# Performance work log

Measured on AMD Instinct MI355X. Metric: run time of the kernel, lower is better.

The kernel has to match this reference:

```python
import jax, jax.numpy as jnp
import numpy as np

N_HEAD = 12
HEAD_SIZE = 64  # 768 / 12
SCALE = 1.0 / np.sqrt(HEAD_SIZE)


def setup_inputs() -> dict:
    key = jax.random.key(0)
    k1, k2, k3 = jax.random.split(key, 3)
    B, T, C = 8, 1024, 768
    x = jax.random.normal(k1, (B, T, C), dtype=jnp.float32)
    W_attn = jax.random.normal(k2, (C, 3 * C), dtype=jnp.float32) * 0.02
    b_attn = jax.random.normal(k3, (3 * C,), dtype=jnp.float32) * 0.02
    return {"x": x, "W_attn": W_attn, "b_attn": b_attn}


def reference(x, W_attn, b_attn):
    B, T, C = x.shape
    hs = C // N_HEAD
    qkv = x @ W_attn + b_attn                      # [B, T, 3C]
    q, k, v = jnp.split(qkv, 3, axis=-1)
    # [B, nh, T, hs]
    q = q.reshape(B, T, N_HEAD, hs).transpose(0, 2, 1, 3)
    k = k.reshape(B, T, N_HEAD, hs).transpose(0, 2, 1, 3)
    v = v.reshape(B, T, N_HEAD, hs).transpose(0, 2, 1, 3)
    scores = jnp.einsum('bhqd,bhkd->bhqk', q, k) * SCALE
    causal = jnp.tril(jnp.ones((T, T), dtype=bool))  # [T, T]
    # masked positions get -inf then relu -> 0; equivalent to where(mask, relu, 0)
    att = jnp.where(causal, jax.nn.relu(scores), 0.0)
    y = jnp.einsum('bhqk,bhkd->bhqd', att, v)      # [B, nh, T, hs]
    return y.transpose(0, 2, 1, 3).reshape(B, T, C)
```

## Files before the change

kernel.cpp:

```cpp
#include <hip/hip_runtime.h>
#include <stdint.h>

typedef __bf16 bf16;
typedef __attribute__((ext_vector_type(8))) __bf16 bf16x8;
typedef __attribute__((ext_vector_type(4))) __bf16 bf16x4;
typedef __attribute__((ext_vector_type(4))) float  f32x4;

#define ATT_SCALE 0.125f

__device__ __forceinline__ void async16(void* lds, const void* g) {
  __builtin_amdgcn_global_load_lds(
      (__attribute__((address_space(1))) void*)(void*)g,
      (__attribute__((address_space(3))) void*)lds,
      16, 0, 0);
}

__global__ void convert_x_kernel(const float* __restrict__ x, bf16* __restrict__ y) {
  size_t i = ((size_t)blockIdx.x * 256 + threadIdx.x) * 8;
  float4 a = *(const float4*)(x + i);
  float4 b = *(const float4*)(x + i + 4);
  bf16x8 o;
  o[0] = (bf16)a.x; o[1] = (bf16)a.y; o[2] = (bf16)a.z; o[3] = (bf16)a.w;
  o[4] = (bf16)b.x; o[5] = (bf16)b.y; o[6] = (bf16)b.z; o[7] = (bf16)b.w;
  *(bf16x8*)(y + i) = o;
}

__global__ void transpose_w_kernel(const float* __restrict__ W, bf16* __restrict__ Wt) {
  __shared__ float tile[32][33];
  int tx = threadIdx.x, ty = threadIdx.y;
  int n0 = blockIdx.x * 32, k0 = blockIdx.y * 32;
#pragma unroll
  for (int r = 0; r < 4; ++r)
    tile[ty + r * 8][tx] = W[(size_t)(k0 + ty + r * 8) * 2304 + n0 + tx];
  __syncthreads();
#pragma unroll
  for (int r = 0; r < 4; ++r)
    Wt[(size_t)(n0 + ty + r * 8) * 768 + k0 + tx] = (bf16)tile[tx][ty + r * 8];
}

__global__ void qkv_gemm_kernel(const bf16* __restrict__ A, const bf16* __restrict__ Bw,
                                const float* __restrict__ bias,
                                bf16* __restrict__ Qo, bf16* __restrict__ Ko,
                                bf16* __restrict__ Vo) {
  __shared__ __align__(16) char lds[65536];

  const int tid  = threadIdx.x;
  const int wave = tid >> 6, lane = tid & 63;
  const int quad = lane >> 4, mn = lane & 15;
  const int wr = wave >> 1, wc = wave & 1;
  const int m0 = blockIdx.y * 128;
  const int n0 = blockIdx.x * 128;

  f32x4 acc[4][4] = {};

  const int lrow = lane >> 3;
  const int cg   = (lane & 7) ^ lrow;

  auto stage = [&](int kt, char* buf) {
    char* Al = buf;
    char* Bl = buf + 16384;
#pragma unroll
    for (int u = 0; u < 4; ++u) {
      const int t   = wave * 4 + u;
      const int row = t * 8 + lrow;
      async16(Al + t * 1024 + lane * 16,
              A  + (size_t)(m0 + row) * 768 + kt + cg * 8);
      async16(Bl + t * 1024 + lane * 16,
              Bw + (size_t)(n0 + row) * 768 + kt + cg * 8);
    }
  };

  stage(0, lds);
  int p = 0;
  for (int kt = 0; kt < 768; kt += 64) {
    __syncthreads();
    if (kt + 64 < 768) stage(kt + 64, lds + (p ^ 1) * 32768);
    char* Al = lds + p * 32768;
    char* Bl = Al + 16384;

#pragma unroll
    for (int s = 0; s < 2; ++s) {
      bf16x8 af[4], bfr[4];
      const int csw = ((s * 4 + quad) ^ (mn & 7)) * 16;
#pragma unroll
      for (int i = 0; i < 4; ++i) {
        af[i]  = *(const bf16x8*)(Al + (wr * 64 + i * 16 + mn) * 128 + csw);
        bfr[i] = *(const bf16x8*)(Bl + (wc * 64 + i * 16 + mn) * 128 + csw);
      }
#pragma unroll
      for (int i = 0; i < 4; ++i)
#pragma unroll
        for (int j = 0; j < 4; ++j)
          acc[i][j] = __builtin_amdgcn_mfma_f32_16x16x32_bf16(af[i], bfr[j], acc[i][j], 0, 0, 0);
    }
    p ^= 1;
  }

  const int ng    = n0 + wc * 64;
  const int third = ng / 768;
  const int nmod  = ng % 768;
  const float sc  = (third == 0) ? ATT_SCALE : 1.0f;
#pragma unroll
  for (int ct = 0; ct < 4; ++ct) {
    int n = nmod + ct * 16 + mn;
    int h = n >> 6, d = n & 63;
    float bv = bias[third * 768 + n];
#pragma unroll
    for (int rt = 0; rt < 4; ++rt) {
      int m  = m0 + wr * 64 + rt * 16 + quad * 4;
      int b  = m >> 10, t0 = m & 1023;
      size_t bh = (size_t)b * 12 + h;
      if (third == 2) {
        bf16x4 pk;
#pragma unroll
        for (int r = 0; r < 4; ++r) pk[r] = (bf16)(acc[rt][ct][r] + bv);
        *(bf16x4*)(Vo + (bh * 64 + d) * 1024 + t0) = pk;
      } else {
        bf16* dst = (third == 0 ? Qo : Ko) + (bh * 1024 + t0) * 64 + d;
#pragma unroll
        for (int r = 0; r < 4; ++r) dst[(size_t)r * 64] = (bf16)((acc[rt][ct][r] + bv) * sc);
      }
    }
  }
}

__global__ __launch_bounds__(256, 3)
void attn_kernel(const bf16* __restrict__ Q, const bf16* __restrict__ K,
                 const bf16* __restrict__ Vt, float* __restrict__ out) {
  __shared__ __align__(16) char lds[51200];
  char* ldsS = lds + 32768;

  const int tid  = threadIdx.x;
  const int wave = tid >> 6, lane = tid & 63;
  const int quad = lane >> 4, mn = lane & 15;
  const int bh  = blockIdx.x;
  const int qta = blockIdx.y;
  const int qtb = 15 - qta;
  const int qa0 = qta * 64, qb0 = qtb * 64;

  const bf16* Qg  = Q  + (size_t)bh * 65536;
  const bf16* Kg0 = K  + (size_t)bh * 65536;
  const bf16* Vg0 = Vt + (size_t)bh * 65536;

  bf16x8 qfA[2], qfB[2];
  {
    const bf16* ra = Qg + (size_t)(qa0 + wave * 16 + mn) * 64;
    qfA[0] = *(const bf16x8*)(ra + quad * 8);
    qfA[1] = *(const bf16x8*)(ra + 32 + quad * 8);
    const bf16* rb = Qg + (size_t)(qb0 + wave * 16 + mn) * 64;
    qfB[0] = *(const bf16x8*)(rb + quad * 8);
    qfB[1] = *(const bf16x8*)(rb + 32 + quad * 8);
  }

  f32x4 yA[4] = {}, yB[4] = {};

  const int lrow = lane >> 3;
  const int cg   = (lane & 7) ^ lrow;

  auto stageKV = [&](int j, char* buf) {
#pragma unroll
    for (int u2 = 0; u2 < 2; ++u2) {
      const int u   = wave * 2 + u2;
      const int row = u * 8 + lrow;
      async16(buf + u * 1024 + lane * 16,
              Kg0 + (size_t)(j * 64 + row) * 64 + cg * 8);
      async16(buf + 8192 + u * 1024 + lane * 16,
              Vg0 + (size_t)row * 1024 + j * 64 + cg * 8);
    }
  };

  stageKV(0, lds);
  for (int j = 0; j <= qtb; ++j) {
    __syncthreads();
    if (j < qtb) stageKV(j + 1, lds + ((j + 1) & 1) * 16384);
    char* bK = lds + (j & 1) * 16384;
    char* bV = bK + 8192;

    bf16x8 kf[4][2], vf[4][2];
    const int sw = mn & 7;
#pragma unroll
    for (int ct = 0; ct < 4; ++ct) {
      const int ro = (ct * 16 + mn) * 128;
      kf[ct][0] = *(const bf16x8*)(bK + ro + ((quad)     ^ sw) * 16);
      kf[ct][1] = *(const bf16x8*)(bK + ro + ((4 + quad) ^ sw) * 16);
      vf[ct][0] = *(const bf16x8*)(bV + ro + ((quad)     ^ sw) * 16);
      vf[ct][1] = *(const bf16x8*)(bV + ro + ((4 + quad) ^ sw) * 16);
    }

    auto do_half = [&](const bf16x8* qf, f32x4* y, int half, int qrow, bool diag) {
#pragma unroll
      for (int ct = 0; ct < 4; ++ct) {
        f32x4 a = {};
        a = __builtin_amdgcn_mfma_f32_16x16x32_bf16(kf[ct][0], qf[0], a, 0, 0, 0);
        a = __builtin_amdgcn_mfma_f32_16x16x32_bf16(kf[ct][1], qf[1], a, 0, 0, 0);
        const int kkg = j * 64 + ct * 16 + quad * 4;
        bf16x4 pk;
#pragma unroll
        for (int r = 0; r < 4; ++r) {
          float v = a[r];
          v = v > 0.f ? v : 0.f;
          if (diag && kkg + r > qrow) v = 0.f;
          pk[r] = (bf16)v;
        }
        *(bf16x4*)(ldsS + (half * 64 + wave * 16 + mn) * 144 + (ct * 16 + quad * 4) * 2) = pk;
      }
#pragma unroll
      for (int kb = 0; kb < 2; ++kb) {
        bf16x8 sf = *(const bf16x8*)(ldsS + (half * 64 + wave * 16 + mn) * 144 + kb * 64 + quad * 16);
#pragma unroll
        for (int ct = 0; ct < 4; ++ct)
          y[ct] = __builtin_amdgcn_mfma_f32_16x16x32_bf16(sf, vf[ct][kb], y[ct], 0, 0, 0);
      }
    };

    if (j <= qta) do_half(qfA, yA, 0, qa0 + wave * 16 + mn, j == qta);
    do_half(qfB, yB, 1, qb0 + wave * 16 + mn, j == qtb);
  }

  const int b = bh / 12, h = bh % 12;
  {
    float* ob = out + ((size_t)b * 1024 + qa0 + wave * 16 + quad * 4) * 768 + h * 64;
#pragma unroll
    for (int ct = 0; ct < 4; ++ct)
#pragma unroll
      for (int r = 0; r < 4; ++r)
        ob[(size_t)r * 768 + ct * 16 + mn] = yA[ct][r];
  }
  {
    float* ob = out + ((size_t)b * 1024 + qb0 + wave * 16 + quad * 4) * 768 + h * 64;
#pragma unroll
    for (int ct = 0; ct < 4; ++ct)
#pragma unroll
      for (int r = 0; r < 4; ++r)
        ob[(size_t)r * 768 + ct * 16 + mn] = yB[ct][r];
  }
}

extern "C" void kernel_launch(void* const* d_in, const int* in_sizes, int n_in,
                              void* d_out, int out_size, void* d_ws, size_t ws_size,
                              hipStream_t stream) {
  const float* x    = (const float*)d_in[0];
  const float* W    = (const float*)d_in[1];
  const float* bias = (const float*)d_in[2];
  float* out = (float*)d_out;

  char* ws = (char*)d_ws;
  bf16* xb = (bf16*)(ws);
  bf16* Wt = (bf16*)(ws + 12582912);
  bf16* Qb = (bf16*)(ws + 16121856);
  bf16* Kb = (bf16*)(ws + 28704768);
  bf16* Vb = (bf16*)(ws + 41287680);

  convert_x_kernel<<<3072, 256, 0, stream>>>(x, xb);
  transpose_w_kernel<<<dim3(72, 24), dim3(32, 8), 0, stream>>>(W, Wt);
  qkv_gemm_kernel<<<dim3(18, 64), 256, 0, stream>>>(xb, Wt, bias, Qb, Kb, Vb);
  attn_kernel<<<dim3(96, 8), 256, 0, stream>>>(Qb, Kb, Vb, out);
}
```

Measured before the change: 149.7 us.

## Load attention K/V fragments directly into double-buffered registers instead of LDS

Replaces the async global-to-LDS staging of K and V tiles with direct per-wave global loads into register fragments, double-buffered across iterations. This removes the per-tile block barrier and LDS staging traffic, and shrinks LDS use to the score scratch buffer. In exchange each wave reloads the same K/V data from cache, uses more registers, and the launch bound lowers occupancy from 3 to 2 blocks.

```diff
diff --git a/kernel.cpp b/kernel.cpp
--- a/kernel.cpp
+++ b/kernel.cpp
@@ -124,11 +124,10 @@
   }
 }
 
-__global__ __launch_bounds__(256, 3)
+__global__ __launch_bounds__(256, 2)
 void attn_kernel(const bf16* __restrict__ Q, const bf16* __restrict__ K,
                  const bf16* __restrict__ Vt, float* __restrict__ out) {
-  __shared__ __align__(16) char lds[51200];
-  char* ldsS = lds + 32768;
+  __shared__ __align__(16) char ldsS[18432];
 
   const int tid  = threadIdx.x;
   const int wave = tid >> 6, lane = tid & 63;
@@ -154,39 +153,21 @@
 
   f32x4 yA[4] = {}, yB[4] = {};
 
-  const int lrow = lane >> 3;
-  const int cg   = (lane & 7) ^ lrow;
-
-  auto stageKV = [&](int j, char* buf) {
-#pragma unroll
-    for (int u2 = 0; u2 < 2; ++u2) {
-      const int u   = wave * 2 + u2;
-      const int row = u * 8 + lrow;
-      async16(buf + u * 1024 + lane * 16,
-              Kg0 + (size_t)(j * 64 + row) * 64 + cg * 8);
-      async16(buf + 8192 + u * 1024 + lane * 16,
-              Vg0 + (size_t)row * 1024 + j * 64 + cg * 8);
+  auto loadT = [&](int j, bf16x8 (&kf)[4][2], bf16x8 (&vf)[4][2]) {
+    const bf16* Kj = Kg0 + (size_t)j * 4096;
+    const bf16* Vj = Vg0 + j * 64;
+#pragma unroll
+    for (int ct = 0; ct < 4; ++ct) {
+      const bf16* kr = Kj + (ct * 16 + mn) * 64 + quad * 8;
+      kf[ct][0] = *(const bf16x8*)(kr);
+      kf[ct][1] = *(const bf16x8*)(kr + 32);
+      const bf16* vr = Vj + (size_t)(ct * 16 + mn) * 1024 + quad * 8;
+      vf[ct][0] = *(const bf16x8*)(vr);
+      vf[ct][1] = *(const bf16x8*)(vr + 32);
     }
   };
 
-  stageKV(0, lds);
-  for (int j = 0; j <= qtb; ++j) {
-    __syncthreads();
-    if (j < qtb) stageKV(j + 1, lds + ((j + 1) & 1) * 16384);
-    char* bK = lds + (j & 1) * 16384;
-    char* bV = bK + 8192;
-
-    bf16x8 kf[4][2], vf[4][2];
-    const int sw = mn & 7;
-#pragma unroll
-    for (int ct = 0; ct < 4; ++ct) {
-      const int ro = (ct * 16 + mn) * 128;
-      kf[ct][0] = *(const bf16x8*)(bK + ro + ((quad)     ^ sw) * 16);
-      kf[ct][1] = *(const bf16x8*)(bK + ro + ((4 + quad) ^ sw) * 16);
-      vf[ct][0] = *(const bf16x8*)(bV + ro + ((quad)     ^ sw) * 16);
-      vf[ct][1] = *(const bf16x8*)(bV + ro + ((4 + quad) ^ sw) * 16);
-    }
-
+  auto compute = [&](const bf16x8 (&kf)[4][2], const bf16x8 (&vf)[4][2], int j) {
     auto do_half = [&](const bf16x8* qf, f32x4* y, int half, int qrow, bool diag) {
 #pragma unroll
       for (int ct = 0; ct < 4; ++ct) {
@@ -212,9 +193,19 @@
           y[ct] = __builtin_amdgcn_mfma_f32_16x16x32_bf16(sf, vf[ct][kb], y[ct], 0, 0, 0);
       }
     };
-
     if (j <= qta) do_half(qfA, yA, 0, qa0 + wave * 16 + mn, j == qta);
     do_half(qfB, yB, 1, qb0 + wave * 16 + mn, j == qtb);
+  };
+
+  bf16x8 kfA[4][2], vfA[4][2], kfB[4][2], vfB[4][2];
+  loadT(0, kfA, vfA);
+  for (int jj = 0; jj <= qtb; jj += 2) {
+    if (jj + 1 <= qtb) loadT(jj + 1, kfB, vfB);
+    compute(kfA, vfA, jj);
+    if (jj + 1 <= qtb) {
+      if (jj + 2 <= qtb) loadT(jj + 2, kfA, vfA);
+      compute(kfB, vfB, jj + 1);
+    }
   }
 
   const int b = bh / 12, h = bh % 12;
```

Result: slower. 194.7 us (+30.1%).

## Merge prep kernels, XOR-swizzle score LDS, and interleave QK/SV of both halves

Applied to the files above, without the earlier changes.

Merges the x conversion and W transpose into one launch, with a block-index branch, to save a kernel launch. In the attention kernel, the padded score scratch (row stride 144) becomes an unpadded 128-byte stride with an XOR swizzle, shrinking LDS from 51200 to 49152 bytes. The QK products for both query tiles are now issued before either SV product, giving the scheduler more independent MFMA work between the LDS writes and reads. The risk is that the new swizzle could cause bank conflicts on the 8-byte writes.

```diff
diff --git a/kernel.cpp b/kernel.cpp
--- a/kernel.cpp
+++ b/kernel.cpp
@@ -15,27 +15,30 @@
       16, 0, 0);
 }
 
-__global__ void convert_x_kernel(const float* __restrict__ x, bf16* __restrict__ y) {
-  size_t i = ((size_t)blockIdx.x * 256 + threadIdx.x) * 8;
-  float4 a = *(const float4*)(x + i);
-  float4 b = *(const float4*)(x + i + 4);
-  bf16x8 o;
-  o[0] = (bf16)a.x; o[1] = (bf16)a.y; o[2] = (bf16)a.z; o[3] = (bf16)a.w;
-  o[4] = (bf16)b.x; o[5] = (bf16)b.y; o[6] = (bf16)b.z; o[7] = (bf16)b.w;
-  *(bf16x8*)(y + i) = o;
-}
-
-__global__ void transpose_w_kernel(const float* __restrict__ W, bf16* __restrict__ Wt) {
+__global__ void prep_kernel(const float* __restrict__ x, bf16* __restrict__ y,
+                            const float* __restrict__ W, bf16* __restrict__ Wt) {
   __shared__ float tile[32][33];
-  int tx = threadIdx.x, ty = threadIdx.y;
-  int n0 = blockIdx.x * 32, k0 = blockIdx.y * 32;
-#pragma unroll
-  for (int r = 0; r < 4; ++r)
-    tile[ty + r * 8][tx] = W[(size_t)(k0 + ty + r * 8) * 2304 + n0 + tx];
-  __syncthreads();
-#pragma unroll
-  for (int r = 0; r < 4; ++r)
-    Wt[(size_t)(n0 + ty + r * 8) * 768 + k0 + tx] = (bf16)tile[tx][ty + r * 8];
+  const int tid = threadIdx.x;
+  if (blockIdx.x < 3072) {
+    size_t i = ((size_t)blockIdx.x * 256 + tid) * 8;
+    float4 a = *(const float4*)(x + i);
+    float4 b = *(const float4*)(x + i + 4);
+    bf16x8 o;
+    o[0] = (bf16)a.x; o[1] = (bf16)a.y; o[2] = (bf16)a.z; o[3] = (bf16)a.w;
+    o[4] = (bf16)b.x; o[5] = (bf16)b.y; o[6] = (bf16)b.z; o[7] = (bf16)b.w;
+    *(bf16x8*)(y + i) = o;
+  } else {
+    const int bid = blockIdx.x - 3072;
+    const int tx = tid & 31, ty = tid >> 5;
+    const int n0 = (bid % 72) * 32, k0 = (bid / 72) * 32;
+#pragma unroll
+    for (int r = 0; r < 4; ++r)
+      tile[ty + r * 8][tx] = W[(size_t)(k0 + ty + r * 8) * 2304 + n0 + tx];
+    __syncthreads();
+#pragma unroll
+    for (int r = 0; r < 4; ++r)
+      Wt[(size_t)(n0 + ty + r * 8) * 768 + k0 + tx] = (bf16)tile[tx][ty + r * 8];
+  }
 }
 
 __global__ void qkv_gemm_kernel(const bf16* __restrict__ A, const bf16* __restrict__ Bw,
@@ -127,7 +130,7 @@
 __global__ __launch_bounds__(256, 3)
 void attn_kernel(const bf16* __restrict__ Q, const bf16* __restrict__ K,
                  const bf16* __restrict__ Vt, float* __restrict__ out) {
-  __shared__ __align__(16) char lds[51200];
+  __shared__ __align__(16) char lds[49152];
   char* ldsS = lds + 32768;
 
   const int tid  = threadIdx.x;
@@ -169,6 +172,8 @@
     }
   };
 
+  const int srow = (wave * 16 + mn) * 128;
+
   stageKV(0, lds);
   for (int j = 0; j <= qtb; ++j) {
     __syncthreads();
@@ -187,7 +192,7 @@
       vf[ct][1] = *(const bf16x8*)(bV + ro + ((4 + quad) ^ sw) * 16);
     }
 
-    auto do_half = [&](const bf16x8* qf, f32x4* y, int half, int qrow, bool diag) {
+    auto qk_half = [&](const bf16x8* qf, int half, int qrow, bool diag) {
 #pragma unroll
       for (int ct = 0; ct < 4; ++ct) {
         f32x4 a = {};
@@ -202,19 +207,25 @@
           if (diag && kkg + r > qrow) v = 0.f;
           pk[r] = (bf16)v;
         }
-        *(bf16x4*)(ldsS + (half * 64 + wave * 16 + mn) * 144 + (ct * 16 + quad * 4) * 2) = pk;
-      }
+        *(bf16x4*)(ldsS + half * 8192 + srow +
+                   (((ct * 4 + quad) ^ (sw << 1)) & 15) * 8) = pk;
+      }
+    };
+    auto sv_half = [&](f32x4* y, int half) {
 #pragma unroll
       for (int kb = 0; kb < 2; ++kb) {
-        bf16x8 sf = *(const bf16x8*)(ldsS + (half * 64 + wave * 16 + mn) * 144 + kb * 64 + quad * 16);
+        bf16x8 sf = *(const bf16x8*)(ldsS + half * 8192 + srow +
+                                     ((kb * 4 + quad) ^ sw) * 16);
 #pragma unroll
         for (int ct = 0; ct < 4; ++ct)
           y[ct] = __builtin_amdgcn_mfma_f32_16x16x32_bf16(sf, vf[ct][kb], y[ct], 0, 0, 0);
       }
     };
 
-    if (j <= qta) do_half(qfA, yA, 0, qa0 + wave * 16 + mn, j == qta);
-    do_half(qfB, yB, 1, qb0 + wave * 16 + mn, j == qtb);
+    if (j <= qta) qk_half(qfA, 0, qa0 + wave * 16 + mn, j == qta);
+    qk_half(qfB, 1, qb0 + wave * 16 + mn, j == qtb);
+    if (j <= qta) sv_half(yA, 0);
+    sv_half(yB, 1);
   }
 
   const int b = bh / 12, h = bh % 12;
@@ -251,8 +262,7 @@
   bf16* Kb = (bf16*)(ws + 28704768);
   bf16* Vb = (bf16*)(ws + 41287680);
 
-  convert_x_kernel<<<3072, 256, 0, stream>>>(x, xb);
-  transpose_w_kernel<<<dim3(72, 24), dim3(32, 8), 0, stream>>>(W, Wt);
+  prep_kernel<<<4800, 256, 0, stream>>>(x, xb, W, Wt);
   qkv_gemm_kernel<<<dim3(18, 64), 256, 0, stream>>>(xb, Wt, bias, Qb, Kb, Vb);
   attn_kernel<<<dim3(96, 8), 256, 0, stream>>>(Qb, Kb, Vb, out);
 }
```

New measurement: 145.8 us. 2.6% less time.
